# Performance work log

Measured on AMD Instinct MI355X. Metric: run time of the kernel, lower is better.

Reference implementation:

```python
import jax, jax.numpy as jnp
import numpy as np

N_NODES = 50000
N_EDGES = 800000
N_REL = 16
N_GRAPHS = 64
IN_DIM = 128
HID = 128
FC = 256
N_CLASSES = 16


def setup_inputs() -> dict:
    key = jax.random.key(0)
    ks = jax.random.split(key, 16)
    h = jax.random.normal(ks[0], (N_NODES, IN_DIM), dtype=jnp.float32)
    src = jax.random.randint(ks[1], (N_EDGES,), 0, N_NODES, dtype=jnp.int32)
    dst = jax.random.randint(ks[2], (N_EDGES,), 0, N_NODES, dtype=jnp.int32)
    rel_types = jax.random.randint(ks[3], (N_EDGES,), 0, N_REL, dtype=jnp.int32)
    graph_ids = jnp.sort(jax.random.randint(ks[4], (N_NODES,), 0, N_GRAPHS, dtype=jnp.int32))
    s1 = 1.0 / np.sqrt(IN_DIM)
    s2 = 1.0 / np.sqrt(HID)
    # RGCN layer 1: per-relation weights, self-loop weight, bias
    W1 = jax.random.normal(ks[5], (N_REL, IN_DIM, HID), dtype=jnp.float32) * s1
    Ws1 = jax.random.normal(ks[6], (IN_DIM, HID), dtype=jnp.float32) * s1
    b1 = jnp.zeros((HID,), dtype=jnp.float32)
    # RGCN layer 2
    W2 = jax.random.normal(ks[7], (N_REL, HID, HID), dtype=jnp.float32) * s2
    Ws2 = jax.random.normal(ks[8], (HID, HID), dtype=jnp.float32) * s2
    b2 = jnp.zeros((HID,), dtype=jnp.float32)
    # FC layer after mean pooling
    Wfc = jax.random.normal(ks[9], (HID, FC), dtype=jnp.float32) * s2
    bfc = jnp.zeros((FC,), dtype=jnp.float32)
    # classify head
    Wc = jax.random.normal(ks[10], (FC, N_CLASSES), dtype=jnp.float32) * (1.0 / np.sqrt(FC))
    bc = jnp.zeros((N_CLASSES,), dtype=jnp.float32)
    return dict(h=h, src=src, dst=dst, rel_types=rel_types, graph_ids=graph_ids,
                W1=W1, Ws1=Ws1, b1=b1, W2=W2, Ws2=Ws2, b2=b2,
                Wfc=Wfc, bfc=bfc, Wc=Wc, bc=bc)


def _rel_graph_conv(h, W, Ws, b, src, dst, rel):
    # dgl RelGraphConv (regularizer=None, self_loop=True, bias=True):
    # out[v] = sum_{e:(u->v)} W[rel_e] @ h[u] + Ws @ h[v] + b
    hW = jnp.einsum('ni,rio->rno', h, W)            # [R, N, out]
    msg = hW[rel, src]                               # [E, out] gather per edge
    agg = jax.ops.segment_sum(msg, dst, num_segments=N_NODES)
    return agg + h @ Ws + b


def _mean_nodes(h, graph_ids):
    sums = jax.ops.segment_sum(h, graph_ids, num_segments=N_GRAPHS)      # [G, D]
    cnts = jax.ops.segment_sum(jnp.ones((h.shape[0], 1), h.dtype), graph_ids,
                               num_segments=N_GRAPHS)                    # [G, 1]
    return sums / jnp.maximum(cnts, 1.0)


def reference(h, src, dst, rel_types, graph_ids,
              W1, Ws1, b1, W2, Ws2, b2, Wfc, bfc, Wc, bc):
    h = h.astype(jnp.float32)
    h = jax.nn.relu(_rel_graph_conv(h, W1, Ws1, b1, src, dst, rel_types))
    h = jax.nn.relu(_rel_graph_conv(h, W2, Ws2, b2, src, dst, rel_types))
    hg = _mean_nodes(h, graph_ids)                   # [G, HID]
    hg = jax.nn.relu(hg @ Wfc + bfc)                 # [G, FC]
    return jax.nn.softmax(hg @ Wc + bc, axis=1)      # [G, n_classes]
```

## Files before the change

kernel.cpp:

```cpp
#include <hip/hip_runtime.h>
#include <hip/hip_bf16.h>

#define N_NODES   50000
#define N_PAD     50048
#define N_EDGES   800000
#define N_REL     16
#define N_GRAPHS  64
#define DIM       128
#define FC_DIM    256
#define N_CLASSES 16

#define SB        50176
#define NBINS_P   (16 * SB)
#define NBLK_PP   784
#define NCOARSE   782
#define NCH       98
#define CHSZ      8192
#define POOL_CH   64
#define NBVIRT    13328
#define GRID_A    1024

#define WS_MARK   0
#define WS_HG     802816
#define WS_CNT    835584
#define WS_SRCOF  835840
#define MEMSET_SZ 4038912
#define WS_BLKH   4038912
#define WS_COFS   4345600
#define WS_PARTP  4348928
#define WS_BLKB   4352256
#define WS_RELB   4355584
#define WS_CIDMAP 4355840
#define WS_RTMP   7567104
#define WS_RECS   10767104
#define WS_OFFSD  13967104
#define WS_X1     14167552
#define WS_X2     26979840
#define WS_AGG    39792128
#define WS_WB     52604416
#define WS_T      53718528

#define XW_TOTAL  (N_PAD * DIM + 2 * 17 * 16384)

typedef __attribute__((ext_vector_type(8))) short bf16x8;
typedef __attribute__((ext_vector_type(4))) float f32x4;

__device__ __forceinline__ void atomAddF(float* p, float v) {
#if defined(__gfx90a__) || defined(__gfx942__) || defined(__gfx950__)
    unsafeAtomicAdd(p, v);
#else
    atomicAdd(p, v);
#endif
}

__device__ __forceinline__ float bf2f(unsigned int u) {
    union { float f; unsigned int i; } x; x.i = u << 16; return x.f;
}
__device__ __forceinline__ unsigned short f2bf(float f) {
    union { float f; unsigned int u; } x; x.f = f;
    unsigned int r = x.u + 0x7fff + ((x.u >> 16) & 1);
    return (unsigned short)(r >> 16);
}
__device__ __forceinline__ void accum8(float* qa, uint4 u) {
    qa[0] += bf2f(u.x & 0xffff); qa[1] += bf2f(u.x >> 16);
    qa[2] += bf2f(u.y & 0xffff); qa[3] += bf2f(u.y >> 16);
    qa[4] += bf2f(u.z & 0xffff); qa[5] += bf2f(u.z >> 16);
    qa[6] += bf2f(u.w & 0xffff); qa[7] += bf2f(u.w >> 16);
}
__device__ __forceinline__ void pack16(const float* qa, unsigned short* dst) {
    #pragma unroll
    for (int j = 0; j < 2; ++j) {
        uint4 w;
        w.x = ((unsigned int)f2bf(qa[j*8+1]) << 16) | f2bf(qa[j*8+0]);
        w.y = ((unsigned int)f2bf(qa[j*8+3]) << 16) | f2bf(qa[j*8+2]);
        w.z = ((unsigned int)f2bf(qa[j*8+5]) << 16) | f2bf(qa[j*8+4]);
        w.w = ((unsigned int)f2bf(qa[j*8+7]) << 16) | f2bf(qa[j*8+6]);
        ((uint4*)dst)[j] = w;
    }
}

__global__ void k_convXW(const float* __restrict__ h, unsigned short* __restrict__ x1,
                         const float* __restrict__ W1, const float* __restrict__ Ws1,
                         const float* __restrict__ W2, const float* __restrict__ Ws2,
                         unsigned short* __restrict__ Wb) {
    int id = blockIdx.x * blockDim.x + threadIdx.x;
    if (id < N_PAD * DIM) {
        int v = id >> 7;
        x1[id] = (v < N_NODES) ? f2bf(h[id]) : (unsigned short)0;
    } else {
        int t = id - N_PAD * DIM;
        int l = t / 278528, rem = t % 278528;
        int r = rem >> 14, rr = rem & 16383;
        int n = rr >> 7, k = rr & 127;
        const float* W  = l ? W2 : W1;
        const float* Ws = l ? Ws2 : Ws1;
        float v = (r < 16) ? W[r * 16384 + k * 128 + n] : Ws[k * 128 + n];
        Wb[t] = f2bf(v);
    }
}

__global__ __launch_bounds__(256) void k_h1(
    const int* __restrict__ src, const int* __restrict__ dst, const int* __restrict__ rel,
    unsigned char* __restrict__ mark, int* __restrict__ blockHist)
{
    __shared__ int hl[NCOARSE];
    int b = blockIdx.x, t = threadIdx.x;
    for (int i = t; i < NCOARSE; i += 256) hl[i] = 0;
    __syncthreads();
    int e0 = b * CHSZ;
    int eend = min(e0 + CHSZ, N_EDGES);
    for (int e = e0 + t; e < eend; e += 256) {
        int d = dst[e];
        mark[rel[e] * SB + src[e]] = 1;
        atomicAdd(&hl[d >> 6], 1);
    }
    __syncthreads();
    for (int i = t; i < NCOARSE; i += 256) blockHist[b * NCOARSE + i] = hl[i];
}

__global__ void k_cscan(int* __restrict__ blockHist, int* __restrict__ coarseOffs) {
    __shared__ int s1[1024], s2[1024];
    int t = threadIdx.x;
    int tot = 0;
    if (t < NCOARSE) {
        int run = 0;
        for (int b = 0; b < NCH; ++b) {
            int v = blockHist[b * NCOARSE + t];
            blockHist[b * NCOARSE + t] = run;
            run += v;
        }
        tot = run;
    }
    s1[t] = tot; __syncthreads();
    int* cur = s1; int* nxt = s2;
    for (int o = 1; o < 1024; o <<= 1) {
        nxt[t] = cur[t] + ((t >= o) ? cur[t - o] : 0);
        __syncthreads();
        int* tmp = cur; cur = nxt; nxt = tmp;
    }
    if (t < NCOARSE) {
        int base = cur[t] - tot;
        coarseOffs[t] = base;
        for (int b = 0; b < NCH; ++b) blockHist[b * NCOARSE + t] += base;
    }
    if (t == NCOARSE) coarseOffs[NCOARSE] = cur[NCOARSE - 1];
}

__global__ void k_scanPA(const unsigned int* __restrict__ markU, int* __restrict__ partP) {
    __shared__ int red[256];
    int b = blockIdx.x, t = threadIdx.x;
    unsigned int u = markU[b * 256 + t];
    red[t] = (int)((u & 1) + ((u >> 8) & 1) + ((u >> 16) & 1) + ((u >> 24) & 1));
    __syncthreads();
    for (int o = 128; o > 0; o >>= 1) {
        if (t < o) red[t] += red[t + o];
        __syncthreads();
    }
    if (t == 0) partP[b] = red[0];
}

__global__ void k_scanPB(const int* __restrict__ partP, int* __restrict__ blkB,
                         int* __restrict__ relB) {
    __shared__ int s1[784], s2[784];
    __shared__ int tot[16], rbase[17];
    int t = threadIdx.x;
    int rel = t / 49, pos = t - rel * 49;
    int v = (t < 784) ? partP[t] : 0;
    if (t < 784) s1[t] = v;
    __syncthreads();
    int* cur = s1; int* nxt = s2;
    for (int o = 1; o < 64; o <<= 1) {
        if (t < 784) nxt[t] = cur[t] + ((pos >= o) ? cur[t - o] : 0);
        __syncthreads();
        int* tmp = cur; cur = nxt; nxt = tmp;
    }
    if (t < 784 && pos == 48) tot[rel] = cur[t];
    __syncthreads();
    if (t == 0) {
        int base = 0;
        for (int r = 0; r < 16; ++r) { rbase[r] = base; base += (tot[r] + 63) & ~63; }
        rbase[16] = base;
    }
    __syncthreads();
    if (t < 784) blkB[t] = rbase[rel] + cur[t] - v;
    if (t < 17)  relB[t] = rbase[t];
}

__global__ void k_scanPC(const unsigned int* __restrict__ markU, const int* __restrict__ blkB,
                         int* __restrict__ cidMap, int* __restrict__ srcOf) {
    __shared__ int s1[256], s2[256];
    int b = blockIdx.x, t = threadIdx.x;
    unsigned int u = markU[b * 256 + t];
    int f0 = (int)(u & 1), f1 = (int)((u >> 8) & 1);
    int f2 = (int)((u >> 16) & 1), f3 = (int)((u >> 24) & 1);
    int sum = f0 + f1 + f2 + f3;
    s1[t] = sum; __syncthreads();
    int* cur = s1; int* nxt = s2;
    for (int o = 1; o < 256; o <<= 1) {
        nxt[t] = cur[t] + ((t >= o) ? cur[t - o] : 0);
        __syncthreads();
        int* tmp = cur; cur = nxt; nxt = tmp;
    }
    int cid = blkB[b] + cur[t] - sum;
    int rel = b / 49;
    int key0 = b * 1024 + t * 4;
    int srcBase = key0 - rel * SB;
    if (f0) { cidMap[key0]     = cid; srcOf[cid] = srcBase;     cid++; }
    if (f1) { cidMap[key0 + 1] = cid; srcOf[cid] = srcBase + 1; cid++; }
    if (f2) { cidMap[key0 + 2] = cid; srcOf[cid] = srcBase + 2; cid++; }
    if (f3) { cidMap[key0 + 3] = cid; srcOf[cid] = srcBase + 3; cid++; }
}

__global__ __launch_bounds__(256) void k_scat1(
    const int* __restrict__ src, const int* __restrict__ dst, const int* __restrict__ rel,
    const int* __restrict__ cidMap, const int* __restrict__ blockHist,
    unsigned int* __restrict__ rtmp)
{
    __shared__ int baseL[NCOARSE];
    __shared__ int hl[NCOARSE];
    int b = blockIdx.x, t = threadIdx.x;
    for (int i = t; i < NCOARSE; i += 256) { baseL[i] = blockHist[b * NCOARSE + i]; hl[i] = 0; }
    __syncthreads();
    int e0 = b * CHSZ;
    int eend = min(e0 + CHSZ, N_EDGES);
    for (int e = e0 + t; e < eend; e += 256) {
        int d = dst[e];
        int cid = cidMap[rel[e] * SB + src[e]];
        int c = d >> 6;
        int rank = atomicAdd(&hl[c], 1);
        rtmp[baseL[c] + rank] = ((unsigned int)cid << 6) | (unsigned int)(d & 63);
    }
}

__global__ __launch_bounds__(256) void k_p2(
    const unsigned int* __restrict__ rtmp, const int* __restrict__ coarseOffs,
    unsigned int* __restrict__ recs, int* __restrict__ offsD)
{
    __shared__ int cntL[64], exclL[65], cur2[64];
    int i = blockIdx.x, t = threadIdx.x;
    int segB = coarseOffs[i], segE = coarseOffs[i + 1];
    if (t < 64) { cntL[t] = 0; cur2[t] = 0; }
    __syncthreads();
    for (int e = segB + t; e < segE; e += 256)
        atomicAdd(&cntL[rtmp[e] & 63u], 1);
    __syncthreads();
    if (t == 0) {
        int run = segB;
        #pragma unroll
        for (int d = 0; d < 64; ++d) { exclL[d] = run; run += cntL[d]; }
        exclL[64] = run;
    }
    __syncthreads();
    if (t < 64) offsD[i * 64 + t] = exclL[t];
    if (t == 64) offsD[i * 64 + 64] = exclL[64];
    for (int e = segB + t; e < segE; e += 256) {
        unsigned int r = rtmp[e];
        int d = (int)(r & 63u);
        int rank = atomicAdd(&cur2[d], 1);
        recs[exclL[d] + rank] = r >> 6;
    }
}

__global__ __launch_bounds__(256) void k_phaseA(
    const unsigned short* __restrict__ x, const unsigned short* __restrict__ Wb,
    const int* __restrict__ srcOf, const int* __restrict__ relB,
    unsigned short* __restrict__ T)
{
    __shared__ __attribute__((aligned(16))) unsigned short Xs[64 * 136];
    __shared__ __attribute__((aligned(16))) unsigned short Cs[64 * 136];
    __shared__ int sRB[17];

    int tid = threadIdx.x;
    if (tid < 17) sRB[tid] = relB[tid];
    __syncthreads();
    int rtot = sRB[16];

    int row = tid >> 2, c0 = tid & 3;

    auto tileInfo = [&](int vb, int& trow0, int& tr) -> bool {
        int chunk = vb / 136;
        int lane = vb - chunk * 136;
        int r = lane >> 3;
        int i = chunk * 8 + (lane & 7);
        int base, cnt;
        if (r == 16) { base = rtot; cnt = N_PAD / 64; }
        else         { base = sRB[r]; cnt = (sRB[r + 1] - base) >> 6; }
        if (i >= cnt) return false;
        trow0 = base + i * 64; tr = r;
        return true;
    };

    int vb = blockIdx.x;
    int cur_row0, cur_r;
    while (vb < NBVIRT && !tileInfo(vb, cur_row0, cur_r)) vb += gridDim.x;
    if (vb >= NBVIRT) return;

    uint4 g0, g1, g2, g3;
    {
        int sr = (cur_r == 16) ? (cur_row0 - rtot + row) : srcOf[cur_row0 + row];
        const uint4* xp = (const uint4*)(x + (size_t)sr * DIM);
        g0 = xp[c0]; g1 = xp[c0 + 4]; g2 = xp[c0 + 8]; g3 = xp[c0 + 12];
    }

    int w = tid >> 6, l = tid & 63;
    int nl = l & 15, q = l >> 4;

    while (true) {
        {
            uint4* lp = (uint4*)(&Xs[row * 136]);
            lp[c0] = g0; lp[c0 + 4] = g1; lp[c0 + 8] = g2; lp[c0 + 12] = g3;
        }
        bf16x8 Bf[2][4];
        {
            const unsigned short* wr = Wb + cur_r * 16384;
            #pragma unroll
            for (int nt = 0; nt < 2; ++nt) {
                int n = w * 32 + nt * 16 + nl;
                #pragma unroll
                for (int kc = 0; kc < 4; ++kc)
                    Bf[nt][kc] = *(const bf16x8*)(wr + n * 128 + kc * 32 + q * 8);
            }
        }
        int nvb = vb + gridDim.x;
        int nxt_row0 = 0, nxt_r = 0;
        while (nvb < NBVIRT && !tileInfo(nvb, nxt_row0, nxt_r)) nvb += gridDim.x;
        bool nhave = (nvb < NBVIRT);
        if (nhave) {
            int sr = (nxt_r == 16) ? (nxt_row0 - rtot + row) : srcOf[nxt_row0 + row];
            const uint4* xp = (const uint4*)(x + (size_t)sr * DIM);
            g0 = xp[c0]; g1 = xp[c0 + 4]; g2 = xp[c0 + 8]; g3 = xp[c0 + 12];
        }
        __syncthreads();
        #pragma unroll
        for (int m = 0; m < 4; ++m) {
            f32x4 a0 = {0.f, 0.f, 0.f, 0.f}, a1 = {0.f, 0.f, 0.f, 0.f};
            #pragma unroll
            for (int kc = 0; kc < 4; ++kc) {
                bf16x8 a = *(const bf16x8*)(&Xs[(m * 16 + nl) * 136 + kc * 32 + q * 8]);
                a0 = __builtin_amdgcn_mfma_f32_16x16x32_bf16(a, Bf[0][kc], a0, 0, 0, 0);
                a1 = __builtin_amdgcn_mfma_f32_16x16x32_bf16(a, Bf[1][kc], a1, 0, 0, 0);
            }
            int colb = w * 32 + nl;
            #pragma unroll
            for (int reg = 0; reg < 4; ++reg) {
                int row2 = m * 16 + q * 4 + reg;
                int sw = ((row2 >> 3) & 1) << 4;
                Cs[row2 * 136 + (colb ^ sw)]        = f2bf(a0[reg]);
                Cs[row2 * 136 + ((colb + 16) ^ sw)] = f2bf(a1[reg]);
            }
        }
        __syncthreads();
        {
            unsigned short* Tb = T + (size_t)cur_row0 * DIM;
            #pragma unroll
            for (int it = 0; it < 4; ++it) {
                int c = tid + it * 256;
                int rw = c >> 4, k8 = c & 15;
                int sw = ((rw >> 3) & 1) << 4;
                uint4 vv = *(const uint4*)(&Cs[rw * 136 + ((k8 * 8) ^ sw)]);
                *(uint4*)(Tb + rw * DIM + k8 * 8) = vv;
            }
        }
        if (!nhave) break;
        vb = nvb; cur_row0 = nxt_row0; cur_r = nxt_r;
    }
}

__global__ __launch_bounds__(256) void k_phaseB(
    const unsigned short* __restrict__ T, const unsigned int* __restrict__ recs,
    const int* __restrict__ offsD, const int* __restrict__ relB,
    const float* __restrict__ bias,
    unsigned short* __restrict__ aggOut, int relu)
{
    __shared__ int sOffs[33];
    __shared__ float sBias[128];
    __shared__ int sSelf;
    int tid = threadIdx.x;
    int v0 = blockIdx.x * 32;
    if (tid < 33) sOffs[tid] = offsD[v0 + tid];
    if (tid == 40) sSelf = relB[16];
    if (tid >= 64 && tid < 96) ((float4*)sBias)[tid - 64] = ((const float4*)bias)[tid - 64];
    __syncthreads();

    int g = tid >> 3, s = tid & 7;
    int dst = v0 + g;
    float qa[16];
    #pragma unroll
    for (int i = 0; i < 16; ++i) qa[i] = sBias[s * 16 + i];

    int beg = sOffs[g], end = sOffs[g + 1];
    int e = beg;
    for (; e + 3 < end; e += 4) {
        unsigned int c0 = recs[e], c1 = recs[e+1], c2 = recs[e+2], c3 = recs[e+3];
        const uint4* t0 = (const uint4*)(T + (size_t)c0 * DIM + s * 16);
        const uint4* t1 = (const uint4*)(T + (size_t)c1 * DIM + s * 16);
        const uint4* t2 = (const uint4*)(T + (size_t)c2 * DIM + s * 16);
        const uint4* t3 = (const uint4*)(T + (size_t)c3 * DIM + s * 16);
        uint4 a0 = t0[0], a1 = t0[1], b0 = t1[0], b1 = t1[1];
        uint4 cc0 = t2[0], cc1 = t2[1], d0 = t3[0], d1 = t3[1];
        accum8(qa, a0); accum8(qa + 8, a1);
        accum8(qa, b0); accum8(qa + 8, b1);
        accum8(qa, cc0); accum8(qa + 8, cc1);
        accum8(qa, d0); accum8(qa + 8, d1);
    }
    for (; e < end; ++e) {
        unsigned int c = recs[e];
        const uint4* tp = (const uint4*)(T + (size_t)c * DIM + s * 16);
        uint4 u0 = tp[0], u1 = tp[1];
        accum8(qa, u0); accum8(qa + 8, u1);
    }
    {
        const uint4* tp = (const uint4*)(T + (size_t)(sSelf + dst) * DIM + s * 16);
        uint4 u0 = tp[0], u1 = tp[1];
        accum8(qa, u0); accum8(qa + 8, u1);
    }

    if (relu) {
        #pragma unroll
        for (int i = 0; i < 16; ++i) qa[i] = fmaxf(qa[i], 0.f);
    }
    pack16(qa, aggOut + (size_t)dst * DIM + s * 16);
}

__global__ void k_pool(const unsigned short* __restrict__ agg2, const int* __restrict__ gids,
                       float* __restrict__ hg_sum, int* __restrict__ cnt)
{
    int d  = threadIdx.x;
    int n0 = blockIdx.x * POOL_CH;
    int nend = min(n0 + POOL_CH, N_NODES);
    if (n0 >= N_NODES) return;
    int curg = gids[n0];
    float run = 0.f;
    for (int n = n0; n < nend; ++n) {
        int g = gids[n];
        if (g != curg) { atomAddF(&hg_sum[curg*DIM + d], run); run = 0.f; curg = g; }
        run += fmaxf(bf2f((unsigned int)agg2[n*DIM + d]), 0.f);
    }
    atomAddF(&hg_sum[curg*DIM + d], run);
    if (d == 0) {
        int cg = gids[n0]; int rl = 0;
        for (int n = n0; n < nend; ++n) {
            int g = gids[n];
            if (g != cg) { atomicAdd(&cnt[cg], rl); rl = 0; cg = g; }
            rl++;
        }
        atomicAdd(&cnt[cg], rl);
    }
}

__global__ __launch_bounds__(256) void k_head(
    const float* __restrict__ hg_sum, const int* __restrict__ cnt,
    const float* __restrict__ Wfc, const float* __restrict__ bfc,
    const float* __restrict__ Wc, const float* __restrict__ bc,
    float* __restrict__ out)
{
    int g = blockIdx.x, t = threadIdx.x;
    __shared__ float hgl[DIM];
    __shared__ float fcl[FC_DIM];
    __shared__ float lg[N_CLASSES];
    if (t < DIM) {
        float c = (float)max(cnt[g], 1);
        hgl[t] = hg_sum[g*DIM + t] / c;
    }
    __syncthreads();
    {
        float sv = bfc[t];
        #pragma unroll 4
        for (int k = 0; k < DIM; ++k) sv += hgl[k] * Wfc[k*FC_DIM + t];
        fcl[t] = fmaxf(sv, 0.f);
    }
    __syncthreads();
    if (t < N_CLASSES) {
        float lgt = bc[t];
        #pragma unroll 4
        for (int k = 0; k < FC_DIM; ++k) lgt += fcl[k] * Wc[k*N_CLASSES + t];
        lg[t] = lgt;
    }
    __syncthreads();
    if (t < N_CLASSES) {
        float m = lg[0];
        #pragma unroll
        for (int c = 1; c < N_CLASSES; ++c) m = fmaxf(m, lg[c]);
        float sden = 0.f;
        #pragma unroll
        for (int c = 0; c < N_CLASSES; ++c) sden += expf(lg[c] - m);
        out[g*N_CLASSES + t] = expf(lg[t] - m) / sden;
    }
}

extern "C" void kernel_launch(void* const* d_in, const int* in_sizes, int n_in,
                              void* d_out, int out_size, void* d_ws, size_t ws_size,
                              hipStream_t stream)
{
    const float* h   = (const float*)d_in[0];
    const int*   src = (const int*)d_in[1];
    const int*   dst = (const int*)d_in[2];
    const int*   rel = (const int*)d_in[3];
    const int*   gid = (const int*)d_in[4];
    const float* W1  = (const float*)d_in[5];
    const float* Ws1 = (const float*)d_in[6];
    const float* b1  = (const float*)d_in[7];
    const float* W2  = (const float*)d_in[8];
    const float* Ws2 = (const float*)d_in[9];
    const float* b2  = (const float*)d_in[10];
    const float* Wfc = (const float*)d_in[11];
    const float* bfc = (const float*)d_in[12];
    const float* Wc  = (const float*)d_in[13];
    const float* bc  = (const float*)d_in[14];
    float* out = (float*)d_out;

    char* ws = (char*)d_ws;
    unsigned char* mark = (unsigned char*)(ws + WS_MARK);
    float* hgsum = (float*)(ws + WS_HG);
    int*   cnt   = (int*)(ws + WS_CNT);
    int*   srcOf = (int*)(ws + WS_SRCOF);
    int*   blkH  = (int*)(ws + WS_BLKH);
    int*   cOffs = (int*)(ws + WS_COFS);
    int*   partP = (int*)(ws + WS_PARTP);
    int*   blkB  = (int*)(ws + WS_BLKB);
    int*   relB  = (int*)(ws + WS_RELB);
    int*   cidMap= (int*)(ws + WS_CIDMAP);
    unsigned int* rtmp = (unsigned int*)(ws + WS_RTMP);
    unsigned int* recs = (unsigned int*)(ws + WS_RECS);
    int*   offsD = (int*)(ws + WS_OFFSD);
    unsigned short* x1  = (unsigned short*)(ws + WS_X1);
    unsigned short* x2  = (unsigned short*)(ws + WS_X2);
    unsigned short* agg = (unsigned short*)(ws + WS_AGG);
    unsigned short* Wb  = (unsigned short*)(ws + WS_WB);
    unsigned short* T   = (unsigned short*)(ws + WS_T);

    hipMemsetAsync(mark, 0, MEMSET_SZ, stream);

    k_convXW<<<XW_TOTAL / 256, 256, 0, stream>>>(h, x1, W1, Ws1, W2, Ws2, Wb);
    k_h1<<<NCH, 256, 0, stream>>>(src, dst, rel, mark, blkH);

    k_cscan<<<1, 1024, 0, stream>>>(blkH, cOffs);
    k_scanPA<<<NBLK_PP, 256, 0, stream>>>((const unsigned int*)mark, partP);
    k_scanPB<<<1, 1024, 0, stream>>>(partP, blkB, relB);
    k_scanPC<<<NBLK_PP, 256, 0, stream>>>((const unsigned int*)mark, blkB, cidMap, srcOf);

    k_scat1<<<NCH, 256, 0, stream>>>(src, dst, rel, cidMap, blkH, rtmp);
    k_p2<<<NCOARSE, 256, 0, stream>>>(rtmp, cOffs, recs, offsD);

    k_phaseA<<<GRID_A, 256, 0, stream>>>(x1, Wb, srcOf, relB, T);
    k_phaseB<<<N_PAD / 32, 256, 0, stream>>>(T, recs, offsD, relB, b1, x2, 1);
    k_phaseA<<<GRID_A, 256, 0, stream>>>(x2, Wb + 17 * 16384, srcOf, relB, T);
    k_phaseB<<<N_PAD / 32, 256, 0, stream>>>(T, recs, offsD, relB, b2, agg, 0);

    k_pool<<<(N_PAD + POOL_CH - 1) / POOL_CH, 128, 0, stream>>>(agg, gid, hgsum, cnt);
    k_head<<<N_GRAPHS, 256, 0, stream>>>(hgsum, cnt, Wfc, bfc, Wc, bc, out);
}
```

Before: 433.9 us.

## Merge preprocessing kernels and parallelize coarse histogram scan across blocks

Merges the edge histogram/mark pass with the bf16 conversion of features and weights into one launch using block-index dispatch. Replaces the single-block serial coarse scan with a per-bin column scan spread over many blocks, fused with the mark popcount pass. The final cross-bin scan runs in a second block of the relation-scan kernel, and the scatter kernel now adds the coarse offsets itself. This cuts launch count and removes a serial 98-step loop, but puts unrelated work into shared kernels, which may affect occupancy and scheduling.

```diff
diff --git a/kernel.cpp b/kernel.cpp
--- a/kernel.cpp
+++ b/kernel.cpp
@@ -19,6 +19,9 @@
 #define POOL_CH   64
 #define NBVIRT    13328
 #define GRID_A    1024
+
+#define NBLK_CX   27200
+#define XW_TOTAL  (N_PAD * DIM + 2 * 17 * 16384)
 
 #define WS_MARK   0
 #define WS_HG     802816
@@ -40,8 +43,6 @@
 #define WS_WB     52604416
 #define WS_T      53718528
 
-#define XW_TOTAL  (N_PAD * DIM + 2 * 17 * 16384)
-
 typedef __attribute__((ext_vector_type(8))) short bf16x8;
 typedef __attribute__((ext_vector_type(4))) float f32x4;
 
@@ -79,111 +80,123 @@
     }
 }
 
-__global__ void k_convXW(const float* __restrict__ h, unsigned short* __restrict__ x1,
-                         const float* __restrict__ W1, const float* __restrict__ Ws1,
-                         const float* __restrict__ W2, const float* __restrict__ Ws2,
-                         unsigned short* __restrict__ Wb) {
-    int id = blockIdx.x * blockDim.x + threadIdx.x;
-    if (id < N_PAD * DIM) {
-        int v = id >> 7;
-        x1[id] = (v < N_NODES) ? f2bf(h[id]) : (unsigned short)0;
+__global__ __launch_bounds__(256) void k_h1cx(
+    const int* __restrict__ src, const int* __restrict__ dst, const int* __restrict__ rel,
+    unsigned char* __restrict__ mark, int* __restrict__ blockHist,
+    const float* __restrict__ h, unsigned short* __restrict__ x1,
+    const float* __restrict__ W1, const float* __restrict__ Ws1,
+    const float* __restrict__ W2, const float* __restrict__ Ws2,
+    unsigned short* __restrict__ Wb)
+{
+    __shared__ int hl[NCOARSE];
+    int t = threadIdx.x;
+    if (blockIdx.x < NCH) {
+        int b = blockIdx.x;
+        for (int i = t; i < NCOARSE; i += 256) hl[i] = 0;
+        __syncthreads();
+        int e0 = b * CHSZ;
+        int eend = min(e0 + CHSZ, N_EDGES);
+        for (int e = e0 + t; e < eend; e += 256) {
+            int d = dst[e];
+            mark[rel[e] * SB + src[e]] = 1;
+            atomicAdd(&hl[d >> 6], 1);
+        }
+        __syncthreads();
+        for (int i = t; i < NCOARSE; i += 256) blockHist[b * NCOARSE + i] = hl[i];
     } else {
-        int t = id - N_PAD * DIM;
-        int l = t / 278528, rem = t % 278528;
-        int r = rem >> 14, rr = rem & 16383;
-        int n = rr >> 7, k = rr & 127;
-        const float* W  = l ? W2 : W1;
-        const float* Ws = l ? Ws2 : Ws1;
-        float v = (r < 16) ? W[r * 16384 + k * 128 + n] : Ws[k * 128 + n];
-        Wb[t] = f2bf(v);
-    }
-}
-
-__global__ __launch_bounds__(256) void k_h1(
-    const int* __restrict__ src, const int* __restrict__ dst, const int* __restrict__ rel,
-    unsigned char* __restrict__ mark, int* __restrict__ blockHist)
-{
-    __shared__ int hl[NCOARSE];
-    int b = blockIdx.x, t = threadIdx.x;
-    for (int i = t; i < NCOARSE; i += 256) hl[i] = 0;
-    __syncthreads();
-    int e0 = b * CHSZ;
-    int eend = min(e0 + CHSZ, N_EDGES);
-    for (int e = e0 + t; e < eend; e += 256) {
-        int d = dst[e];
-        mark[rel[e] * SB + src[e]] = 1;
-        atomicAdd(&hl[d >> 6], 1);
-    }
-    __syncthreads();
-    for (int i = t; i < NCOARSE; i += 256) blockHist[b * NCOARSE + i] = hl[i];
-}
-
-__global__ void k_cscan(int* __restrict__ blockHist, int* __restrict__ coarseOffs) {
-    __shared__ int s1[1024], s2[1024];
+        int id = (blockIdx.x - NCH) * 256 + t;
+        if (id < N_PAD * DIM) {
+            int v = id >> 7;
+            x1[id] = (v < N_NODES) ? f2bf(h[id]) : (unsigned short)0;
+        } else {
+            int tt = id - N_PAD * DIM;
+            int l = tt / 278528, rem = tt % 278528;
+            int r = rem >> 14, rr = rem & 16383;
+            int n = rr >> 7, k = rr & 127;
+            const float* W  = l ? W2 : W1;
+            const float* Ws = l ? Ws2 : Ws1;
+            float v = (r < 16) ? W[r * 16384 + k * 128 + n] : Ws[k * 128 + n];
+            Wb[tt] = f2bf(v);
+        }
+    }
+}
+
+__global__ __launch_bounds__(256) void k_sA(
+    const unsigned int* __restrict__ markU, int* __restrict__ partP,
+    int* __restrict__ blockHist, int* __restrict__ cOffs)
+{
     int t = threadIdx.x;
-    int tot = 0;
-    if (t < NCOARSE) {
-        int run = 0;
-        for (int b = 0; b < NCH; ++b) {
-            int v = blockHist[b * NCOARSE + t];
-            blockHist[b * NCOARSE + t] = run;
-            run += v;
-        }
-        tot = run;
-    }
-    s1[t] = tot; __syncthreads();
-    int* cur = s1; int* nxt = s2;
-    for (int o = 1; o < 1024; o <<= 1) {
-        nxt[t] = cur[t] + ((t >= o) ? cur[t - o] : 0);
-        __syncthreads();
-        int* tmp = cur; cur = nxt; nxt = tmp;
-    }
-    if (t < NCOARSE) {
-        int base = cur[t] - tot;
-        coarseOffs[t] = base;
-        for (int b = 0; b < NCH; ++b) blockHist[b * NCOARSE + t] += base;
-    }
-    if (t == NCOARSE) coarseOffs[NCOARSE] = cur[NCOARSE - 1];
-}
-
-__global__ void k_scanPA(const unsigned int* __restrict__ markU, int* __restrict__ partP) {
-    __shared__ int red[256];
-    int b = blockIdx.x, t = threadIdx.x;
-    unsigned int u = markU[b * 256 + t];
-    red[t] = (int)((u & 1) + ((u >> 8) & 1) + ((u >> 16) & 1) + ((u >> 24) & 1));
-    __syncthreads();
-    for (int o = 128; o > 0; o >>= 1) {
-        if (t < o) red[t] += red[t + o];
-        __syncthreads();
-    }
-    if (t == 0) partP[b] = red[0];
-}
-
-__global__ void k_scanPB(const int* __restrict__ partP, int* __restrict__ blkB,
-                         int* __restrict__ relB) {
-    __shared__ int s1[784], s2[784];
-    __shared__ int tot[16], rbase[17];
+    if (blockIdx.x < NBLK_PP) {
+        __shared__ int red[256];
+        int b = blockIdx.x;
+        unsigned int u = markU[b * 256 + t];
+        red[t] = (int)((u & 1) + ((u >> 8) & 1) + ((u >> 16) & 1) + ((u >> 24) & 1));
+        __syncthreads();
+        for (int o = 128; o > 0; o >>= 1) {
+            if (t < o) red[t] += red[t + o];
+            __syncthreads();
+        }
+        if (t == 0) partP[b] = red[0];
+    } else {
+        __shared__ int sc[2][128];
+        int i = blockIdx.x - NBLK_PP;
+        int v = 0;
+        if (t < NCH) v = blockHist[t * NCOARSE + i];
+        if (t < 128) sc[0][t] = v;
+        __syncthreads();
+        int cur = 0, nxt = 1;
+        #pragma unroll
+        for (int o = 1; o < 128; o <<= 1) {
+            if (t < 128) sc[nxt][t] = sc[cur][t] + ((t >= o) ? sc[cur][t - o] : 0);
+            __syncthreads();
+            int tmp = cur; cur = nxt; nxt = tmp;
+        }
+        if (t < NCH) blockHist[t * NCOARSE + i] = sc[cur][t] - v;
+        if (t == NCH - 1) cOffs[i] = sc[cur][t];
+    }
+}
+
+__global__ __launch_bounds__(1024) void k_sB(
+    const int* __restrict__ partP, int* __restrict__ blkB, int* __restrict__ relB,
+    int* __restrict__ cOffs)
+{
     int t = threadIdx.x;
-    int rel = t / 49, pos = t - rel * 49;
-    int v = (t < 784) ? partP[t] : 0;
-    if (t < 784) s1[t] = v;
-    __syncthreads();
-    int* cur = s1; int* nxt = s2;
-    for (int o = 1; o < 64; o <<= 1) {
-        if (t < 784) nxt[t] = cur[t] + ((pos >= o) ? cur[t - o] : 0);
-        __syncthreads();
-        int* tmp = cur; cur = nxt; nxt = tmp;
-    }
-    if (t < 784 && pos == 48) tot[rel] = cur[t];
-    __syncthreads();
-    if (t == 0) {
-        int base = 0;
-        for (int r = 0; r < 16; ++r) { rbase[r] = base; base += (tot[r] + 63) & ~63; }
-        rbase[16] = base;
-    }
-    __syncthreads();
-    if (t < 784) blkB[t] = rbase[rel] + cur[t] - v;
-    if (t < 17)  relB[t] = rbase[t];
+    if (blockIdx.x == 0) {
+        __shared__ int s1[784], s2[784];
+        __shared__ int tot[16], rbase[17];
+        int rel = t / 49, pos = t - rel * 49;
+        int v = (t < 784) ? partP[t] : 0;
+        if (t < 784) s1[t] = v;
+        __syncthreads();
+        int* cur = s1; int* nxt = s2;
+        for (int o = 1; o < 64; o <<= 1) {
+            if (t < 784) nxt[t] = cur[t] + ((pos >= o) ? cur[t - o] : 0);
+            __syncthreads();
+            int* tmp = cur; cur = nxt; nxt = tmp;
+        }
+        if (t < 784 && pos == 48) tot[rel] = cur[t];
+        __syncthreads();
+        if (t == 0) {
+            int base = 0;
+            for (int r = 0; r < 16; ++r) { rbase[r] = base; base += (tot[r] + 63) & ~63; }
+            rbase[16] = base;
+        }
+        __syncthreads();
+        if (t < 784) blkB[t] = rbase[rel] + cur[t] - v;
+        if (t < 17)  relB[t] = rbase[t];
+    } else {
+        __shared__ int c1[1024], c2[1024];
+        int v = (t < NCOARSE) ? cOffs[t] : 0;
+        c1[t] = v; __syncthreads();
+        int* cur = c1; int* nxt = c2;
+        for (int o = 1; o < 1024; o <<= 1) {
+            nxt[t] = cur[t] + ((t >= o) ? cur[t - o] : 0);
+            __syncthreads();
+            int* tmp = cur; cur = nxt; nxt = tmp;
+        }
+        if (t < NCOARSE) cOffs[t] = cur[t] - v;
+        if (t == NCOARSE) cOffs[NCOARSE] = cur[NCOARSE - 1];
+    }
 }
 
 __global__ void k_scanPC(const unsigned int* __restrict__ markU, const int* __restrict__ blkB,
@@ -214,12 +227,15 @@
 __global__ __launch_bounds__(256) void k_scat1(
     const int* __restrict__ src, const int* __restrict__ dst, const int* __restrict__ rel,
     const int* __restrict__ cidMap, const int* __restrict__ blockHist,
-    unsigned int* __restrict__ rtmp)
+    const int* __restrict__ cOffs, unsigned int* __restrict__ rtmp)
 {
     __shared__ int baseL[NCOARSE];
     __shared__ int hl[NCOARSE];
     int b = blockIdx.x, t = threadIdx.x;
-    for (int i = t; i < NCOARSE; i += 256) { baseL[i] = blockHist[b * NCOARSE + i]; hl[i] = 0; }
+    for (int i = t; i < NCOARSE; i += 256) {
+        baseL[i] = blockHist[b * NCOARSE + i] + cOffs[i];
+        hl[i] = 0;
+    }
     __syncthreads();
     int e0 = b * CHSZ;
     int eend = min(e0 + CHSZ, N_EDGES);
@@ -531,15 +547,14 @@
 
     hipMemsetAsync(mark, 0, MEMSET_SZ, stream);
 
-    k_convXW<<<XW_TOTAL / 256, 256, 0, stream>>>(h, x1, W1, Ws1, W2, Ws2, Wb);
-    k_h1<<<NCH, 256, 0, stream>>>(src, dst, rel, mark, blkH);
-
-    k_cscan<<<1, 1024, 0, stream>>>(blkH, cOffs);
-    k_scanPA<<<NBLK_PP, 256, 0, stream>>>((const unsigned int*)mark, partP);
-    k_scanPB<<<1, 1024, 0, stream>>>(partP, blkB, relB);
+    k_h1cx<<<NCH + NBLK_CX, 256, 0, stream>>>(src, dst, rel, mark, blkH,
+                                              h, x1, W1, Ws1, W2, Ws2, Wb);
+    k_sA<<<NBLK_PP + NCOARSE, 256, 0, stream>>>((const unsigned int*)mark, partP,
+                                                blkH, cOffs);
+    k_sB<<<2, 1024, 0, stream>>>(partP, blkB, relB, cOffs);
     k_scanPC<<<NBLK_PP, 256, 0, stream>>>((const unsigned int*)mark, blkB, cidMap, srcOf);
 
-    k_scat1<<<NCH, 256, 0, stream>>>(src, dst, rel, cidMap, blkH, rtmp);
+    k_scat1<<<NCH, 256, 0, stream>>>(src, dst, rel, cidMap, blkH, cOffs, rtmp);
     k_p2<<<NCOARSE, 256, 0, stream>>>(rtmp, cOffs, recs, offsD);
 
     k_phaseA<<<GRID_A, 256, 0, stream>>>(x1, Wb, srcOf, relB, T);
```

Result: faster. 408.5 us, median of 2 (-5.9%).
